# Kernel optimization log

Hardware: AMD Instinct MI355X
Metric: run time of the kernel (lower is better)

Reference implementation:

```python
import jax, jax.numpy as jnp
import numpy as np

B, L, DM = 16, 1024, 512
DI, ST, DC, RK, OD = 1024, 16, 4, 32, 128


def setup_inputs() -> dict:
    key = jax.random.key(0)
    ks = jax.random.split(key, 10)
    s = 0.02
    x = jax.random.normal(ks[0], (B, L, DM), dtype=jnp.float32)
    W_in = jax.random.normal(ks[1], (DM, 2 * DI), dtype=jnp.float32) * s
    conv_w = jax.random.normal(ks[2], (DI, DC), dtype=jnp.float32) * 0.2
    conv_b = jax.random.normal(ks[3], (DI,), dtype=jnp.float32) * s
    W_xproj = jax.random.normal(ks[4], (DI, RK + 2 * ST), dtype=jnp.float32) * s
    W_dt = jax.random.normal(ks[5], (RK, DI), dtype=jnp.float32) * s
    b_dt = jax.random.normal(ks[6], (DI,), dtype=jnp.float32) * s
    # S4D-real init: A_log[d, n] = log(n+1)
    A_log = jnp.log(jnp.tile(jnp.arange(1, ST + 1, dtype=jnp.float32)[None, :], (DI, 1)))
    Dp = jnp.ones((DI,), dtype=jnp.float32)
    W_out = jax.random.normal(ks[7], (DI, DM), dtype=jnp.float32) * s
    W_fc = jax.random.normal(ks[8], (L * DM, OD), dtype=jnp.float32) * 0.002
    b_fc = jnp.zeros((OD,), dtype=jnp.float32)
    return {"x": x, "W_in": W_in, "conv_w": conv_w, "conv_b": conv_b,
            "W_xproj": W_xproj, "W_dt": W_dt, "b_dt": b_dt, "A_log": A_log,
            "Dp": Dp, "W_out": W_out, "W_fc": W_fc, "b_fc": b_fc}


def _silu(v):
    return v * jax.nn.sigmoid(v)


def reference(x, W_in, conv_w, conv_b, W_xproj, W_dt, b_dt, A_log, Dp, W_out, W_fc, b_fc):
    b, l, dm = x.shape
    di, dc = conv_w.shape
    rk = W_dt.shape[0]
    st = A_log.shape[1]
    # in_proj -> split into x branch and gate z
    xz = x @ W_in                                # [B,L,2*DI]
    xin, z = jnp.split(xz, 2, axis=-1)
    # causal depthwise conv1d, kernel size dc, truncated to length l
    xp = jnp.pad(xin, ((0, 0), (dc - 1, 0), (0, 0)))
    conv = conv_b
    for j in range(dc):                          # fixed small kernel loop
        conv = conv + xp[:, j:j + l, :] * conv_w[:, j]
    xc = _silu(conv)                             # [B,L,DI]
    # input-dependent dt, B, C
    x_dbl = xc @ W_xproj                         # [B,L,RK+2*ST]
    dt = jax.nn.softplus(x_dbl[..., :rk] @ W_dt + b_dt)   # [B,L,DI]
    Bm = x_dbl[..., rk:rk + st]                  # [B,L,ST]
    Cm = x_dbl[..., rk + st:]                    # [B,L,ST]
    A = -jnp.exp(A_log)                          # [DI,ST]
    # selective scan: h_t = exp(dt_t*A)*h_{t-1} + dt_t*B_t*u_t ; y_t = C_t . h_t
    def step(h, inp):
        dt_t, B_t, C_t, u_t = inp                # [B,DI],[B,ST],[B,ST],[B,DI]
        dA = jnp.exp(dt_t[:, :, None] * A)       # [B,DI,ST]
        h = h * dA + (dt_t * u_t)[:, :, None] * B_t[:, None, :]
        y = jnp.einsum('bds,bs->bd', h, C_t)
        return h, y
    h0 = jnp.zeros((b, di, st), dtype=x.dtype)
    seq = (dt.transpose(1, 0, 2), Bm.transpose(1, 0, 2),
           Cm.transpose(1, 0, 2), xc.transpose(1, 0, 2))
    _, ys = jax.lax.scan(step, h0, seq)          # ys: [L,B,DI]
    y = ys.transpose(1, 0, 2) + Dp * xc          # skip connection
    y = y * _silu(z)                             # gate
    out = y @ W_out                              # [B,L,DM]
    # flatten + fc
    return out.reshape(b, -1) @ W_fc + b_fc      # [B,OD]
```

## Files before the change

### kernel.cpp

```cpp
#include <hip/hip_runtime.h>
#include <hip/hip_bf16.h>

typedef __hip_bfloat16 bf16;
typedef __bf16 bf8v __attribute__((ext_vector_type(8)));
typedef __bf16 bf4v __attribute__((ext_vector_type(4)));
typedef float f4v __attribute__((ext_vector_type(4)));

static __device__ __forceinline__ float tf(const bf16 v) { return __bfloat162float(v); }

static __device__ __forceinline__ float ldv(const void* p, size_t i, bool f32) {
    return f32 ? ((const float*)p)[i] : tf(((const bf16*)p)[i]);
}

static __device__ __forceinline__ void gld_lds16(const bf16* g, __bf16* l) {
    __builtin_amdgcn_global_load_lds(
        (const __attribute__((address_space(1))) void*)g,
        (__attribute__((address_space(3))) void*)l, 16, 0, 0);
}

constexpr int Bz = 16, Lz = 1024, DM = 512, DI = 1024, ST = 16, DC = 4, RK = 32, OD = 128;
constexpr int Mrows = Bz * Lz;
constexpr int XD = RK + 2 * ST;
constexpr int NC = 16, CT = Lz / NC;
constexpr int FC_KC = 512;
constexpr int FC_BLOCKS = (Lz * DM) / FC_KC;
constexpr float LOG2E = 1.4426950408889634f;

__global__ void detect_kernel(const void* __restrict__ xp, int* __restrict__ flag) {
    int i = blockIdx.x * 256 + threadIdx.x;
    const bf16* p = (const bf16*)xp;
    float v = tf(p[(size_t)i * 64]);
    if (!(fabsf(v) < 1e4f)) atomicAdd(flag, 1);
}

__global__ __launch_bounds__(256) void canon_kernel(const void* __restrict__ src,
                                                    bf16* __restrict__ dst,
                                                    const int* __restrict__ flag) {
    const bool f = (*flag != 0);
    size_t base = ((size_t)blockIdx.x * 256 + threadIdx.x) * 8;
    if (!f) {
        *(uint4*)((__bf16*)dst + base) = *(const uint4*)((const bf16*)src + base);
    } else {
        f4v a = *(const f4v*)((const float*)src + base);
        f4v b = *(const f4v*)((const float*)src + base + 4);
        bf8v o;
        #pragma unroll
        for (int j = 0; j < 4; ++j) { o[j] = (__bf16)a[j]; o[j + 4] = (__bf16)b[j]; }
        *(bf8v*)((__bf16*)dst + base) = o;
    }
}

__global__ __launch_bounds__(256) void transpose3_kernel(const void* __restrict__ W0,
                                                         const void* __restrict__ W1,
                                                         const void* __restrict__ W2,
                                                         bf16* __restrict__ T0,
                                                         bf16* __restrict__ T1,
                                                         bf16* __restrict__ T2,
                                                         const int* __restrict__ flag) {
    const bool f = (*flag != 0);
    __shared__ float tile[32][33];
    int bid = blockIdx.x;
    const void* W; bf16* Wt; int K, N, n0, k0;
    if (bid < 1024) {
        W = W0; Wt = T0; K = DM; N = 2 * DI; n0 = (bid & 63) * 32; k0 = (bid >> 6) * 32;
    } else if (bid < 1536) {
        int b = bid - 1024;
        W = W1; Wt = T1; K = DI; N = DM; n0 = (b & 15) * 32; k0 = (b >> 4) * 32;
    } else {
        int b = bid - 1536;
        W = W2; Wt = T2; K = DI; N = XD; n0 = (b & 1) * 32; k0 = (b >> 1) * 32;
    }
    int c = threadIdx.x & 31, r4 = threadIdx.x >> 5;
    #pragma unroll
    for (int i = 0; i < 4; ++i) {
        int r = r4 + i * 8;
        tile[r][c] = ldv(W, (size_t)(k0 + r) * N + n0 + c, f);
    }
    __syncthreads();
    #pragma unroll
    for (int i = 0; i < 4; ++i) {
        int rr = r4 + i * 8;
        Wt[(size_t)(n0 + rr) * K + k0 + c] = __float2bfloat16(tile[c][rr]);
    }
}

template <int MR, int NT, bool SPLIT, bool CF32, int GXL, int KS>
__global__ __launch_bounds__(256) void gemm_bt(const bf16* __restrict__ A, int lda,
                                               const bf16* __restrict__ Bt, int ldb,
                                               void* __restrict__ C0, void* __restrict__ C1,
                                               int ldc, int K) {
    constexpr int MI = (MR == 64) ? 1 : ((NT == 128) ? 4 : 2);
    constexpr int NI = 4;
    constexpr int GX = 1 << GXL;
    __shared__ __align__(16) __bf16 As[2][MR * 32];
    __shared__ __align__(16) __bf16 Bs[2][NT * 32];
    const int tid = threadIdx.x, lane = tid & 63, w = tid >> 6;
    const int l15 = lane & 15, quad = lane >> 4;
    const int wm = (MR == 64) ? w * 16 : ((NT == 128) ? (w >> 1) * 64 : w * 32);
    const int wn = (MR == 64) ? 0 : ((NT == 128) ? (w & 1) * 64 : 0);

    const int nwg = GX * gridDim.y;
    const int bid = blockIdx.y * GX + blockIdx.x;
    const int swz = (bid & 7) * (nwg >> 3) + (bid >> 3);
    const int m0 = (swz >> GXL) * MR, n0 = (swz & (GX - 1)) * NT;

    f4v acc[MI][NI];
    #pragma unroll
    for (int i = 0; i < MI; ++i)
        #pragma unroll
        for (int j = 0; j < NI; ++j)
            #pragma unroll
            for (int r = 0; r < 4; ++r) acc[i][j][r] = 0.f;

    auto stage = [&](int bi, int k0) {
        if constexpr (MR == 128) {
            const int arow = w * 32 + (lane >> 2), ach = lane & 3;
            const bf16* g0 = A + (size_t)(m0 + arow) * lda + k0 + ach * 8;
            gld_lds16(g0, &As[bi][w * 1024 + lane * 8]);
            gld_lds16(g0 + (size_t)16 * lda, &As[bi][w * 1024 + 512 + lane * 8]);
        } else {
            const bf16* g0 = A + (size_t)(m0 + (tid >> 2)) * lda + k0 + (tid & 3) * 8;
            gld_lds16(g0, &As[bi][tid * 8]);
        }
        if constexpr (NT == 128) {
            const int arow = w * 32 + (lane >> 2), ach = lane & 3;
            const bf16* g0 = Bt + (size_t)(n0 + arow) * ldb + k0 + ach * 8;
            gld_lds16(g0, &Bs[bi][w * 1024 + lane * 8]);
            gld_lds16(g0 + (size_t)16 * ldb, &Bs[bi][w * 1024 + 512 + lane * 8]);
        } else {
            const bf16* g0 = Bt + (size_t)(n0 + (tid >> 2)) * ldb + k0 + (tid & 3) * 8;
            gld_lds16(g0, &Bs[bi][tid * 8]);
        }
    };

    const int kslice = K / KS;
    const int kbeg = (KS > 1) ? (int)blockIdx.z * kslice : 0;
    const int kend = kbeg + kslice;

    stage(0, kbeg);
    __syncthreads();
    int cur = 0;
    for (int k0 = kbeg; k0 < kend; k0 += 32) {
        if (k0 + 32 < kend) stage(cur ^ 1, k0 + 32);
        bf8v a[MI], b[NI];
        #pragma unroll
        for (int mi = 0; mi < MI; ++mi)
            a[mi] = *(const bf8v*)&As[cur][(wm + mi * 16 + l15) * 32 + quad * 8];
        #pragma unroll
        for (int ni = 0; ni < NI; ++ni)
            b[ni] = *(const bf8v*)&Bs[cur][(wn + ni * 16 + l15) * 32 + quad * 8];
        #pragma unroll
        for (int mi = 0; mi < MI; ++mi)
            #pragma unroll
            for (int ni = 0; ni < NI; ++ni)
                acc[mi][ni] = __builtin_amdgcn_mfma_f32_16x16x32_bf16(a[mi], b[ni], acc[mi][ni], 0, 0, 0);
        __syncthreads();
        cur ^= 1;
    }
    #pragma unroll
    for (int mi = 0; mi < MI; ++mi)
        #pragma unroll
        for (int ni = 0; ni < NI; ++ni)
            #pragma unroll
            for (int r = 0; r < 4; ++r) {
                int row = m0 + wm + mi * 16 + quad * 4 + r;
                int col = n0 + wn + ni * 16 + l15;
                float v = acc[mi][ni][r];
                if (SPLIT) {
                    if (col < DI) ((bf16*)C0)[(size_t)row * DI + col] = __float2bfloat16(v);
                    else ((bf16*)C1)[(size_t)row * DI + col - DI] =
                             __float2bfloat16(v / (1.f + __expf(-v)));
                } else if (CF32) {
                    if (KS > 1) atomicAdd(&((float*)C0)[(size_t)row * ldc + col], v);
                    else ((float*)C0)[(size_t)row * ldc + col] = v;
                } else {
                    ((bf16*)C0)[(size_t)row * ldc + col] = __float2bfloat16(v);
                }
            }
}

__global__ __launch_bounds__(256) void conv_silu_kernel(const bf16* __restrict__ xin,
                                                        const void* __restrict__ conv_w,
                                                        const void* __restrict__ conv_b,
                                                        bf16* __restrict__ xc,
                                                        const int* __restrict__ flag) {
    const bool f = (*flag != 0);
    int g = blockIdx.x * 256 + threadIdx.x;
    int d = g & (DI - 1);
    int t = (g >> 10) & (Lz - 1);
    int b = g >> 20;
    const bf16* xin_b = xin + (size_t)b * Lz * DI;
    float acc = ldv(conv_b, d, f);
    #pragma unroll
    for (int j = 0; j < DC; ++j) {
        int tt = t + j - (DC - 1);
        if (tt >= 0) acc += tf(xin_b[(size_t)tt * DI + d]) * ldv(conv_w, d * DC + j, f);
    }
    xc[(size_t)g] = __float2bfloat16(acc / (1.f + __expf(-acc)));
}

__global__ __launch_bounds__(256) void scan_pass1(const float* __restrict__ x_dbl,
                                                  const bf16* __restrict__ xc,
                                                  const void* __restrict__ A_log,
                                                  const void* __restrict__ W_dt,
                                                  const void* __restrict__ b_dt,
                                                  _Float16* __restrict__ dtw,
                                                  float* __restrict__ hbuf,
                                                  float* __restrict__ dtsum,
                                                  const int* __restrict__ flag) {
    const bool f = (*flag != 0);
    const int c = blockIdx.x, b = blockIdx.z;
    const int d = blockIdx.y * 256 + threadIdx.x;
    __shared__ float Row[CT][XD];
    #pragma unroll
    for (int i = 0; i < 4; ++i) {
        int idx = threadIdx.x + i * 256;
        int r = idx >> 4, q = idx & 15;
        *(f4v*)&Row[r][q * 4] =
            *(const f4v*)(x_dbl + ((size_t)(b * Lz + c * CT + r)) * XD + q * 4);
    }
    float W[RK];
    #pragma unroll
    for (int k = 0; k < RK; ++k) W[k] = ldv(W_dt, (size_t)k * DI + d, f);
    const float bdt = ldv(b_dt, d, f);
    float A2[ST];
    #pragma unroll
    for (int s = 0; s < ST; ++s) A2[s] = -__expf(ldv(A_log, (size_t)d * ST + s, f)) * LOG2E;
    __syncthreads();
    float h[ST] = {};
    float S = 0.f;
    const bf16* xcp = xc + (size_t)(b * Lz + c * CT) * DI + d;
    _Float16*   dtp = dtw + (size_t)(b * Lz + c * CT) * DI + d;
    for (int t = 0; t < CT; ++t) {
        float acc = bdt;
        #pragma unroll
        for (int k = 0; k < RK; ++k) acc += Row[t][k] * W[k];
        float dtv = (acc > 15.f) ? acc : __logf(1.f + __expf(acc));
        dtp[(size_t)t * DI] = (_Float16)dtv;
        float du  = dtv * tf(xcp[(size_t)t * DI]);
        S += dtv;
        #pragma unroll
        for (int s = 0; s < ST; ++s)
            h[s] = h[s] * exp2f(dtv * A2[s]) + du * Row[t][RK + s];
    }
    float* hp = hbuf + ((size_t)(b * DI + d) * NC + c) * 16;
    #pragma unroll
    for (int s = 0; s < ST; ++s) hp[s] = h[s];
    dtsum[(size_t)(b * DI + d) * NC + c] = S;
}

__global__ __launch_bounds__(256) void scan_prefix(float* __restrict__ hbuf,
                                                   const float* __restrict__ dtsum,
                                                   const void* __restrict__ A_log,
                                                   const int* __restrict__ flag) {
    const bool f = (*flag != 0);
    int g = blockIdx.x * 256 + threadIdx.x;
    int s = g & 15, g2 = g >> 4;
    int d = g2 & (DI - 1);
    float A2 = -__expf(ldv(A_log, (size_t)d * ST + s, f)) * LOG2E;
    float hrun = 0.f;
    for (int c = 0; c < NC; ++c) {
        size_t idx = ((size_t)g2 * NC + c) * 16 + s;
        float he = hbuf[idx];
        float S = dtsum[(size_t)g2 * NC + c];
        hbuf[idx] = hrun;
        hrun = hrun * exp2f(A2 * S) + he;
    }
}

__global__ __launch_bounds__(256) void scan_pass2(const float* __restrict__ x_dbl,
                                                  const _Float16* __restrict__ dtw,
                                                  const bf16* __restrict__ xc,
                                                  const void* __restrict__ A_log,
                                                  const void* __restrict__ Dp,
                                                  bf16* __restrict__ yzs,
                                                  const float* __restrict__ hbuf,
                                                  const int* __restrict__ flag) {
    const bool f = (*flag != 0);
    const int c = blockIdx.x, b = blockIdx.z;
    const int d = blockIdx.y * 256 + threadIdx.x;
    __shared__ float BC[CT][32];
    #pragma unroll
    for (int i = 0; i < 2; ++i) {
        int idx = threadIdx.x + i * 256;
        int r = idx >> 3, q = idx & 7;
        *(f4v*)&BC[r][q * 4] =
            *(const f4v*)(x_dbl + ((size_t)(b * Lz + c * CT + r)) * XD + RK + q * 4);
    }
    float A2[ST];
    #pragma unroll
    for (int s = 0; s < ST; ++s) A2[s] = -__expf(ldv(A_log, (size_t)d * ST + s, f)) * LOG2E;
    float Dp_d = ldv(Dp, d, f);
    __syncthreads();
    float h[ST];
    const float* hp = hbuf + ((size_t)(b * DI + d) * NC + c) * 16;
    #pragma unroll
    for (int s = 0; s < ST; ++s) h[s] = hp[s];
    const _Float16* dtp = dtw + (size_t)(b * Lz + c * CT) * DI + d;
    const bf16*     xcp = xc + (size_t)(b * Lz + c * CT) * DI + d;
    bf16*           yzp = yzs + (size_t)(b * Lz + c * CT) * DI + d;
    for (int t = 0; t < CT; ++t) {
        float dtv = (float)dtp[(size_t)t * DI];
        float u   = tf(xcp[(size_t)t * DI]);
        float du  = dtv * u;
        float p = 0.f;
        #pragma unroll
        for (int s = 0; s < ST; ++s) {
            h[s] = h[s] * exp2f(dtv * A2[s]) + du * BC[t][s];
            p += h[s] * BC[t][16 + s];
        }
        float zz = tf(yzp[(size_t)t * DI]);
        yzp[(size_t)t * DI] = __float2bfloat16((p + Dp_d * u) * zz);
    }
}

__global__ __launch_bounds__(256) void fc_partial_kernel(const bf16* __restrict__ out_pre,
                                                         const void* __restrict__ W_fc,
                                                         float* __restrict__ part,
                                                         const int* __restrict__ flag) {
    const bool f = (*flag != 0);
    __shared__ __align__(16) float u_lds[FC_KC][16];
    const int tid = threadIdx.x;
    const int k0 = blockIdx.x * FC_KC;

    #pragma unroll
    for (int i = 0; i < 4; ++i) {
        int cid = tid + i * 256;
        int b = cid & 15, c8 = cid >> 4;
        bf8v v = *(const bf8v*)&out_pre[(size_t)b * (Lz * DM) + k0 + c8 * 8];
        #pragma unroll
        for (int j = 0; j < 8; ++j) u_lds[c8 * 8 + j][b] = (float)v[j];
    }
    __syncthreads();

    const int ng = tid & 31, kr = tid >> 5;
    f4v acc[16];
    #pragma unroll
    for (int b = 0; b < 16; ++b)
        #pragma unroll
        for (int c = 0; c < 4; ++c) acc[b][c] = 0.f;

    if (f) {
        const float* Wp = (const float*)W_fc + (size_t)(k0 + kr) * OD + ng * 4;
        #pragma unroll 4
        for (int kk = 0; kk < FC_KC; kk += 8) {
            f4v w4 = *(const f4v*)(Wp + (size_t)kk * OD);
            int kl = kk + kr;
            #pragma unroll
            for (int q = 0; q < 4; ++q) {
                f4v uq = *(const f4v*)&u_lds[kl][q * 4];
                #pragma unroll
                for (int c = 0; c < 4; ++c) acc[q * 4 + c] += uq[c] * w4;
            }
        }
    } else {
        const bf16* Wp = (const bf16*)W_fc + (size_t)(k0 + kr) * OD + ng * 4;
        #pragma unroll 4
        for (int kk = 0; kk < FC_KC; kk += 8) {
            bf4v wv = *(const bf4v*)(Wp + (size_t)kk * OD);
            f4v w4;
            #pragma unroll
            for (int c = 0; c < 4; ++c) w4[c] = (float)wv[c];
            int kl = kk + kr;
            #pragma unroll
            for (int q = 0; q < 4; ++q) {
                f4v uq = *(const f4v*)&u_lds[kl][q * 4];
                #pragma unroll
                for (int c = 0; c < 4; ++c) acc[q * 4 + c] += uq[c] * w4;
            }
        }
    }

    #pragma unroll
    for (int b = 0; b < 16; ++b)
        #pragma unroll
        for (int c = 0; c < 4; ++c) acc[b][c] += __shfl_down(acc[b][c], 32);
    __syncthreads();
    f4v* redv = (f4v*)&u_lds[0][0];
    const int w = tid >> 6, lane = tid & 63;
    if (lane < 32) {
        #pragma unroll
        for (int b = 0; b < 16; ++b) redv[(b * 4 + w) * 32 + lane] = acc[b];
    }
    __syncthreads();
    #pragma unroll
    for (int i = 0; i < 2; ++i) {
        int og = tid + i * 256;
        int b = og >> 5, ngo = og & 31;
        f4v s = {0.f, 0.f, 0.f, 0.f};
        #pragma unroll
        for (int w2 = 0; w2 < 4; ++w2) s += redv[(b * 4 + w2) * 32 + ngo];
        *(f4v*)&part[(size_t)blockIdx.x * (Bz * OD) + b * OD + ngo * 4] = s;
    }
}

__global__ __launch_bounds__(256) void fc_reduce_kernel(const float* __restrict__ part,
                                                        float* __restrict__ accb) {
    const int o = blockIdx.x * 256 + threadIdx.x;
    const int s0 = blockIdx.y * (FC_BLOCKS / 16);
    float s = 0.f;
    for (int p = s0; p < s0 + FC_BLOCKS / 16; ++p) s += part[(size_t)p * (Bz * OD) + o];
    atomicAdd(&accb[o], s);
}

__global__ void fc_final_kernel(const float* __restrict__ accbuf,
                                const void* __restrict__ b_fc, void* __restrict__ out,
                                const int* __restrict__ flag) {
    const bool f = (*flag != 0);
    int i = blockIdx.x * 256 + threadIdx.x;
    if (i < Bz * OD) {
        float v = accbuf[i] + ldv(b_fc, i & (OD - 1), f);
        if (f) ((float*)out)[i] = v;
        else   ((bf16*)out)[i]  = __float2bfloat16(v);
    }
}

extern "C" void kernel_launch(void* const* d_in, const int* in_sizes, int n_in,
                              void* d_out, int out_size, void* d_ws, size_t ws_size,
                              hipStream_t stream) {
    const void* x       = d_in[0];
    const void* W_in    = d_in[1];
    const void* conv_w  = d_in[2];
    const void* conv_b  = d_in[3];
    const void* W_xproj = d_in[4];
    const void* W_dt    = d_in[5];
    const void* b_dt    = d_in[6];
    const void* A_log   = d_in[7];
    const void* Dp      = d_in[8];
    const void* W_out   = d_in[9];
    const void* W_fc    = d_in[10];
    const void* b_fc    = d_in[11];

    char* ws = (char*)d_ws;
    bf16*     xin    = (bf16*)(ws);
    _Float16* dtw    = (_Float16*)(ws);
    float*    part   = (float*)(ws);
    bf16*     yzs    = (bf16*)(ws + 33554432ull);
    bf16*     xc     = (bf16*)(ws + 67108864ull);
    float*    x_dbl  = (float*)(ws + 100663296ull);
    bf16*     xb     = (bf16*)(ws + 104857600ull);
    bf16*     outp   = (bf16*)(ws + 104857600ull);
    float*    hbuf   = (float*)(ws + 167772160ull);
    float*    dtsum  = (float*)(ws + 188743680ull);
    bf16*     Wt_in  = (bf16*)(ws + 199229440ull);
    bf16*     Wt_out = (bf16*)(ws + 202375168ull);
    bf16*     Wt_xp  = (bf16*)(ws + 204472320ull);
    float*    accb   = (float*)(ws + 205520896ull);
    int*      flag   = (int*)(ws + 206569472ull);

    dim3 blk(256);
    hipMemsetAsync(flag, 0, 4, stream);
    detect_kernel<<<256, blk, 0, stream>>>(x, flag);
    canon_kernel<<<(Mrows * DM) / 2048, blk, 0, stream>>>(x, xb, flag);
    transpose3_kernel<<<1600, blk, 0, stream>>>(W_in, W_out, W_xproj,
                                                Wt_in, Wt_out, Wt_xp, flag);
    hipLaunchKernelGGL((gemm_bt<128, 128, true, false, 4, 1>),
                       dim3(2 * DI / 128, Mrows / 128), blk, 0, stream,
                       xb, DM, Wt_in, DM, xin, yzs, DI, DM);
    conv_silu_kernel<<<(Mrows * DI) / 256, blk, 0, stream>>>(xin, conv_w, conv_b, xc, flag);
    hipMemsetAsync(x_dbl, 0, (size_t)Mrows * XD * sizeof(float), stream);
    hipLaunchKernelGGL((gemm_bt<64, 64, false, true, 0, 2>),
                       dim3(1, Mrows / 64, 2), blk, 0, stream,
                       xc, DI, Wt_xp, DI, x_dbl, (void*)0, XD, DI);
    scan_pass1<<<dim3(NC, DI / 256, Bz), blk, 0, stream>>>(x_dbl, xc, A_log, W_dt, b_dt,
                                                           dtw, hbuf, dtsum, flag);
    scan_prefix<<<(Bz * DI * ST) / 256, blk, 0, stream>>>(hbuf, dtsum, A_log, flag);
    scan_pass2<<<dim3(NC, DI / 256, Bz), blk, 0, stream>>>(x_dbl, dtw, xc, A_log,
                                                           Dp, yzs, hbuf, flag);
    hipLaunchKernelGGL((gemm_bt<128, 128, false, false, 2, 1>),
                       dim3(DM / 128, Mrows / 128), blk, 0, stream,
                       yzs, DI, Wt_out, DI, outp, (void*)0, DM, DI);
    hipMemsetAsync(accb, 0, Bz * OD * sizeof(float), stream);
    fc_partial_kernel<<<FC_BLOCKS, blk, 0, stream>>>(outp, W_fc, part, flag);
    fc_reduce_kernel<<<dim3((Bz * OD) / 256, 16), blk, 0, stream>>>(part, accb);
    fc_final_kernel<<<(Bz * OD + 255) / 256, blk, 0, stream>>>(accb, b_fc, d_out, flag);
}
```

Baseline: 808.8 us.

## Replace per-state exps with powers of one exp and recompute dt in scan pass2

Both scan passes check at runtime whether A[s] equals (s+1)*A[0] and, if so, compute the decay factors as successive powers of a single exponential instead of 16 separate exps. Pass2 now recomputes dt from x_dbl and W_dt rather than reading an fp16 dt buffer written by pass1, which removes that global round-trip. The x_proj GEMM moves to a 128-row tile without split-K, dropping the zeroing memset. The power chain may accumulate slightly more rounding error, and pass2 takes on extra dot-product work.

```diff
diff --git a/kernel.cpp b/kernel.cpp
--- a/kernel.cpp
+++ b/kernel.cpp
@@ -24,7 +24,6 @@
 constexpr int NC = 16, CT = Lz / NC;
 constexpr int FC_KC = 512;
 constexpr int FC_BLOCKS = (Lz * DM) / FC_KC;
-constexpr float LOG2E = 1.4426950408889634f;
 
 __global__ void detect_kernel(const void* __restrict__ xp, int* __restrict__ flag) {
     int i = blockIdx.x * 256 + threadIdx.x;
@@ -204,7 +203,6 @@
                                                   const void* __restrict__ A_log,
                                                   const void* __restrict__ W_dt,
                                                   const void* __restrict__ b_dt,
-                                                  _Float16* __restrict__ dtw,
                                                   float* __restrict__ hbuf,
                                                   float* __restrict__ dtsum,
                                                   const int* __restrict__ flag) {
@@ -223,25 +221,45 @@
     #pragma unroll
     for (int k = 0; k < RK; ++k) W[k] = ldv(W_dt, (size_t)k * DI + d, f);
     const float bdt = ldv(b_dt, d, f);
-    float A2[ST];
-    #pragma unroll
-    for (int s = 0; s < ST; ++s) A2[s] = -__expf(ldv(A_log, (size_t)d * ST + s, f)) * LOG2E;
+    float A[ST];
+    #pragma unroll
+    for (int s = 0; s < ST; ++s) A[s] = -__expf(ldv(A_log, (size_t)d * ST + s, f));
+    bool fast = true;
+    #pragma unroll
+    for (int s = 0; s < ST; ++s)
+        fast = fast && (fabsf(A[s] - (float)(s + 1) * A[0]) <= 1e-4f * (float)(s + 1));
     __syncthreads();
     float h[ST] = {};
     float S = 0.f;
     const bf16* xcp = xc + (size_t)(b * Lz + c * CT) * DI + d;
-    _Float16*   dtp = dtw + (size_t)(b * Lz + c * CT) * DI + d;
-    for (int t = 0; t < CT; ++t) {
-        float acc = bdt;
-        #pragma unroll
-        for (int k = 0; k < RK; ++k) acc += Row[t][k] * W[k];
-        float dtv = (acc > 15.f) ? acc : __logf(1.f + __expf(acc));
-        dtp[(size_t)t * DI] = (_Float16)dtv;
-        float du  = dtv * tf(xcp[(size_t)t * DI]);
-        S += dtv;
-        #pragma unroll
-        for (int s = 0; s < ST; ++s)
-            h[s] = h[s] * exp2f(dtv * A2[s]) + du * Row[t][RK + s];
+    if (fast) {
+        for (int t = 0; t < CT; ++t) {
+            float acc = bdt;
+            #pragma unroll
+            for (int k = 0; k < RK; ++k) acc += Row[t][k] * W[k];
+            float dtv = (acc > 15.f) ? acc : __logf(1.f + __expf(acc));
+            float du  = dtv * tf(xcp[(size_t)t * DI]);
+            S += dtv;
+            float E = __expf(dtv * A[0]);
+            float P = 1.f;
+            #pragma unroll
+            for (int s = 0; s < ST; ++s) {
+                P *= E;
+                h[s] = h[s] * P + du * Row[t][RK + s];
+            }
+        }
+    } else {
+        for (int t = 0; t < CT; ++t) {
+            float acc = bdt;
+            #pragma unroll
+            for (int k = 0; k < RK; ++k) acc += Row[t][k] * W[k];
+            float dtv = (acc > 15.f) ? acc : __logf(1.f + __expf(acc));
+            float du  = dtv * tf(xcp[(size_t)t * DI]);
+            S += dtv;
+            #pragma unroll
+            for (int s = 0; s < ST; ++s)
+                h[s] = h[s] * __expf(dtv * A[s]) + du * Row[t][RK + s];
+        }
     }
     float* hp = hbuf + ((size_t)(b * DI + d) * NC + c) * 16;
     #pragma unroll
@@ -257,21 +275,22 @@
     int g = blockIdx.x * 256 + threadIdx.x;
     int s = g & 15, g2 = g >> 4;
     int d = g2 & (DI - 1);
-    float A2 = -__expf(ldv(A_log, (size_t)d * ST + s, f)) * LOG2E;
+    float A1 = -__expf(ldv(A_log, (size_t)d * ST + s, f));
     float hrun = 0.f;
     for (int c = 0; c < NC; ++c) {
         size_t idx = ((size_t)g2 * NC + c) * 16 + s;
         float he = hbuf[idx];
         float S = dtsum[(size_t)g2 * NC + c];
         hbuf[idx] = hrun;
-        hrun = hrun * exp2f(A2 * S) + he;
+        hrun = hrun * __expf(A1 * S) + he;
     }
 }
 
 __global__ __launch_bounds__(256) void scan_pass2(const float* __restrict__ x_dbl,
-                                                  const _Float16* __restrict__ dtw,
                                                   const bf16* __restrict__ xc,
                                                   const void* __restrict__ A_log,
+                                                  const void* __restrict__ W_dt,
+                                                  const void* __restrict__ b_dt,
                                                   const void* __restrict__ Dp,
                                                   bf16* __restrict__ yzs,
                                                   const float* __restrict__ hbuf,
@@ -279,38 +298,70 @@
     const bool f = (*flag != 0);
     const int c = blockIdx.x, b = blockIdx.z;
     const int d = blockIdx.y * 256 + threadIdx.x;
-    __shared__ float BC[CT][32];
-    #pragma unroll
-    for (int i = 0; i < 2; ++i) {
+    __shared__ float Row[CT][XD];
+    #pragma unroll
+    for (int i = 0; i < 4; ++i) {
         int idx = threadIdx.x + i * 256;
-        int r = idx >> 3, q = idx & 7;
-        *(f4v*)&BC[r][q * 4] =
-            *(const f4v*)(x_dbl + ((size_t)(b * Lz + c * CT + r)) * XD + RK + q * 4);
-    }
-    float A2[ST];
-    #pragma unroll
-    for (int s = 0; s < ST; ++s) A2[s] = -__expf(ldv(A_log, (size_t)d * ST + s, f)) * LOG2E;
+        int r = idx >> 4, q = idx & 15;
+        *(f4v*)&Row[r][q * 4] =
+            *(const f4v*)(x_dbl + ((size_t)(b * Lz + c * CT + r)) * XD + q * 4);
+    }
+    float W[RK];
+    #pragma unroll
+    for (int k = 0; k < RK; ++k) W[k] = ldv(W_dt, (size_t)k * DI + d, f);
+    const float bdt = ldv(b_dt, d, f);
+    float A[ST];
+    #pragma unroll
+    for (int s = 0; s < ST; ++s) A[s] = -__expf(ldv(A_log, (size_t)d * ST + s, f));
+    bool fast = true;
+    #pragma unroll
+    for (int s = 0; s < ST; ++s)
+        fast = fast && (fabsf(A[s] - (float)(s + 1) * A[0]) <= 1e-4f * (float)(s + 1));
     float Dp_d = ldv(Dp, d, f);
     __syncthreads();
     float h[ST];
     const float* hp = hbuf + ((size_t)(b * DI + d) * NC + c) * 16;
     #pragma unroll
     for (int s = 0; s < ST; ++s) h[s] = hp[s];
-    const _Float16* dtp = dtw + (size_t)(b * Lz + c * CT) * DI + d;
-    const bf16*     xcp = xc + (size_t)(b * Lz + c * CT) * DI + d;
-    bf16*           yzp = yzs + (size_t)(b * Lz + c * CT) * DI + d;
-    for (int t = 0; t < CT; ++t) {
-        float dtv = (float)dtp[(size_t)t * DI];
-        float u   = tf(xcp[(size_t)t * DI]);
-        float du  = dtv * u;
-        float p = 0.f;
-        #pragma unroll
-        for (int s = 0; s < ST; ++s) {
-            h[s] = h[s] * exp2f(dtv * A2[s]) + du * BC[t][s];
-            p += h[s] * BC[t][16 + s];
-        }
-        float zz = tf(yzp[(size_t)t * DI]);
-        yzp[(size_t)t * DI] = __float2bfloat16((p + Dp_d * u) * zz);
+    const bf16* xcp = xc + (size_t)(b * Lz + c * CT) * DI + d;
+    bf16*       yzp = yzs + (size_t)(b * Lz + c * CT) * DI + d;
+    if (fast) {
+        for (int t = 0; t < CT; ++t) {
+            float acc = bdt;
+            #pragma unroll
+            for (int k = 0; k < RK; ++k) acc += Row[t][k] * W[k];
+            float dtv = (acc > 15.f) ? acc : __logf(1.f + __expf(acc));
+            float u   = tf(xcp[(size_t)t * DI]);
+            float du  = dtv * u;
+            float E = __expf(dtv * A[0]);
+            float P = 1.f;
+            float p = 0.f;
+            #pragma unroll
+            for (int s = 0; s < ST; ++s) {
+                P *= E;
+                h[s] = h[s] * P + du * Row[t][RK + s];
+                p += h[s] * Row[t][RK + ST + s];
+            }
+            float zz = tf(yzp[(size_t)t * DI]);
+            yzp[(size_t)t * DI] = __float2bfloat16((p + Dp_d * u) * zz);
+        }
+    } else {
+        for (int t = 0; t < CT; ++t) {
+            float acc = bdt;
+            #pragma unroll
+            for (int k = 0; k < RK; ++k) acc += Row[t][k] * W[k];
+            float dtv = (acc > 15.f) ? acc : __logf(1.f + __expf(acc));
+            float u   = tf(xcp[(size_t)t * DI]);
+            float du  = dtv * u;
+            float p = 0.f;
+            #pragma unroll
+            for (int s = 0; s < ST; ++s) {
+                h[s] = h[s] * __expf(dtv * A[s]) + du * Row[t][RK + s];
+                p += h[s] * Row[t][RK + ST + s];
+            }
+            float zz = tf(yzp[(size_t)t * DI]);
+            yzp[(size_t)t * DI] = __float2bfloat16((p + Dp_d * u) * zz);
+        }
     }
 }
 
@@ -433,7 +484,6 @@
 
     char* ws = (char*)d_ws;
     bf16*     xin    = (bf16*)(ws);
-    _Float16* dtw    = (_Float16*)(ws);
     float*    part   = (float*)(ws);
     bf16*     yzs    = (bf16*)(ws + 33554432ull);
     bf16*     xc     = (bf16*)(ws + 67108864ull);
@@ -458,14 +508,13 @@
                        dim3(2 * DI / 128, Mrows / 128), blk, 0, stream,
                        xb, DM, Wt_in, DM, xin, yzs, DI, DM);
     conv_silu_kernel<<<(Mrows * DI) / 256, blk, 0, stream>>>(xin, conv_w, conv_b, xc, flag);
-    hipMemsetAsync(x_dbl, 0, (size_t)Mrows * XD * sizeof(float), stream);
-    hipLaunchKernelGGL((gemm_bt<64, 64, false, true, 0, 2>),
-                       dim3(1, Mrows / 64, 2), blk, 0, stream,
+    hipLaunchKernelGGL((gemm_bt<128, 64, false, true, 0, 1>),
+                       dim3(1, Mrows / 128), blk, 0, stream,
                        xc, DI, Wt_xp, DI, x_dbl, (void*)0, XD, DI);
     scan_pass1<<<dim3(NC, DI / 256, Bz), blk, 0, stream>>>(x_dbl, xc, A_log, W_dt, b_dt,
-                                                           dtw, hbuf, dtsum, flag);
+                                                           hbuf, dtsum, flag);
     scan_prefix<<<(Bz * DI * ST) / 256, blk, 0, stream>>>(hbuf, dtsum, A_log, flag);
-    scan_pass2<<<dim3(NC, DI / 256, Bz), blk, 0, stream>>>(x_dbl, dtw, xc, A_log,
+    scan_pass2<<<dim3(NC, DI / 256, Bz), blk, 0, stream>>>(x_dbl, xc, A_log, W_dt, b_dt,
                                                            Dp, yzs, hbuf, flag);
     hipLaunchKernelGGL((gemm_bt<128, 128, false, false, 2, 1>),
                        dim3(DM / 128, Mrows / 128), blk, 0, stream,
```

Result: faster. 739.5 us (-8.6%).
